# Kernel optimization log

Measured on AMD Instinct MI355X. Metric: run time of the kernel, lower is better.

Reference implementation:

```python
import jax, jax.numpy as jnp
import numpy as np

H = 24; W = 24; N = H * W            # board tokens
R = 4; BINS = (2 * R + 1) ** 2 + 1    # 82 rel-pos bins (far bin = 81)
G = 2                                  # num_global_tokens
T = N + 1 + G                          # cls + globals + board tokens = 579
D = 256; NH = 8; HD = D // NH
DEPTH = 6; MLP = int(D * 2.0)
B = 16; CIN = 10


def _ln(x, g, b):
    m = jnp.mean(x, axis=-1, keepdims=True)
    v = jnp.mean(jnp.square(x - m), axis=-1, keepdims=True)
    return (x - m) * jax.lax.rsqrt(v + 1e-5) * g + b


def _head(x, g, b, w1, b1, w2, b2):
    h = _ln(x, g, b)
    h = jax.nn.gelu(h @ w1 + b1, approximate=False)
    return h @ w2 + b2


def _forward(obs, input_w, input_b, cls_token, global_tokens, row_embed, col_embed,
             ln1_g, ln1_b, qkv_w, qkv_b, proj_w, proj_b, rel_bias,
             ln2_g, ln2_b, fc1_w, fc1_b, fc2_w, fc2_b,
             norm_g, norm_b,
             pol_ln_g, pol_ln_b, pol_w1, pol_b1, pol_w2, pol_b2,
             val_ln_g, val_ln_b, val_w1, val_b1, val_w2, val_b2,
             rel_idx):
    Bsz = obs.shape[0]
    # _tokens_from_obs: (B, C, H, W) -> (B, N, C); channel order is already [revealed, counts]
    tokens = obs.reshape(Bsz, CIN, N).transpose(0, 2, 1)
    x = tokens @ input_w + input_b                                    # (B, N, D)
    pos = (row_embed[:, None, :] + col_embed[None, :, :]).reshape(N, D)
    x = x + pos
    x = jnp.concatenate([jnp.broadcast_to(cls_token, (Bsz, 1, D)),
                         jnp.broadcast_to(global_tokens, (Bsz, G, D)),
                         x], axis=1)                                   # (B, T, D)
    scale = 1.0 / jnp.sqrt(jnp.float32(HD))

    def block(x, p):
        l1g, l1b, qw, qb, pw, pb, rb, l2g, l2b, f1w, f1b, f2w, f2b = p
        h = _ln(x, l1g, l1b)
        qkv = (h @ qw + qb).reshape(Bsz, T, 3, NH, HD)
        q, k, v = qkv[:, :, 0], qkv[:, :, 1], qkv[:, :, 2]             # (B, T, NH, HD)
        bias = rb[:, rel_idx]                                          # (NH, T, T) gathered bias
        scores = jnp.einsum('bqhd,bkhd->bhqk', q, k) * scale + bias[None]
        probs = jax.nn.softmax(scores, axis=-1)
        o = jnp.einsum('bhqk,bkhd->bqhd', probs, v).reshape(Bsz, T, D)
        x = x + o @ pw + pb
        h2 = _ln(x, l2g, l2b)
        x = x + jax.nn.gelu(h2 @ f1w + f1b, approximate=False) @ f2w + f2b
        return x, None

    params = (ln1_g, ln1_b, qkv_w, qkv_b, proj_w, proj_b, rel_bias,
              ln2_g, ln2_b, fc1_w, fc1_b, fc2_w, fc2_b)
    x, _ = jax.lax.scan(block, x, params)
    x = _ln(x, norm_g, norm_b)
    cls_tok = x[:, 0]
    token_states = x[:, 1:N + 1]   # faithful to source slice (includes the global tokens)
    logits = _head(token_states, pol_ln_g, pol_ln_b, pol_w1, pol_b1, pol_w2, pol_b2)[..., 0]  # (B, N)
    value = _head(cls_tok, val_ln_g, val_ln_b, val_w1, val_b1, val_w2, val_b2)                 # (B, 1)
    return jnp.concatenate([logits, value], axis=1)  # (B, N+1)


def setup_inputs() -> dict:
    keys = iter(jax.random.split(jax.random.key(0), 40))
    def p(shape, s=0.02):
        return jax.random.normal(next(keys), shape, jnp.float32) * s
    # _build_rel_pos_index, embedded into full (T, T) buffer with far_bin elsewhere
    coords = np.stack(np.meshgrid(np.arange(H), np.arange(W), indexing='ij'), -1).reshape(-1, 2)
    rel = coords[:, None, :] - coords[None, :, :]
    far = (np.abs(rel) > R).any(-1)
    rel = np.clip(rel, -R, R) + R
    idx = rel[..., 0] * (2 * R + 1) + rel[..., 1]
    idx = np.where(far, BINS - 1, idx)
    full = np.full((T, T), BINS - 1, np.int32)
    full[1:N + 1, 1:N + 1] = idx
    return {
        'obs': jax.random.normal(next(keys), (B, CIN, H, W), jnp.float32),
        'input_w': p((CIN, D)), 'input_b': jnp.zeros((D,)),
        'cls_token': jnp.zeros((1, 1, D)),
        'global_tokens': jnp.zeros((1, G, D)),
        'row_embed': p((H, D)), 'col_embed': p((W, D)),
        'ln1_g': jnp.ones((DEPTH, D)), 'ln1_b': jnp.zeros((DEPTH, D)),
        'qkv_w': p((DEPTH, D, 3 * D)), 'qkv_b': jnp.zeros((DEPTH, 3 * D)),
        'proj_w': p((DEPTH, D, D)), 'proj_b': jnp.zeros((DEPTH, D)),
        'rel_bias': p((DEPTH, NH, BINS)),
        'ln2_g': jnp.ones((DEPTH, D)), 'ln2_b': jnp.zeros((DEPTH, D)),
        'fc1_w': p((DEPTH, D, MLP)), 'fc1_b': jnp.zeros((DEPTH, MLP)),
        'fc2_w': p((DEPTH, MLP, D)), 'fc2_b': jnp.zeros((DEPTH, D)),
        'norm_g': jnp.ones((D,)), 'norm_b': jnp.zeros((D,)),
        'pol_ln_g': jnp.ones((D,)), 'pol_ln_b': jnp.zeros((D,)),
        'pol_w1': p((D, D)), 'pol_b1': jnp.zeros((D,)),
        'pol_w2': p((D, 1)), 'pol_b2': jnp.zeros((1,)),
        'val_ln_g': jnp.ones((D,)), 'val_ln_b': jnp.zeros((D,)),
        'val_w1': p((D, D)), 'val_b1': jnp.zeros((D,)),
        'val_w2': p((D, 1)), 'val_b2': jnp.zeros((1,)),
        'rel_idx': jnp.asarray(full),
    }


def reference(obs, input_w, input_b, cls_token, global_tokens, row_embed, col_embed,
              ln1_g, ln1_b, qkv_w, qkv_b, proj_w, proj_b, rel_bias,
              ln2_g, ln2_b, fc1_w, fc1_b, fc2_w, fc2_b,
              norm_g, norm_b,
              pol_ln_g, pol_ln_b, pol_w1, pol_b1, pol_w2, pol_b2,
              val_ln_g, val_ln_b, val_w1, val_b1, val_w2, val_b2,
              rel_idx):
    return _forward(obs, input_w, input_b, cls_token, global_tokens, row_embed, col_embed,
                    ln1_g, ln1_b, qkv_w, qkv_b, proj_w, proj_b, rel_bias,
                    ln2_g, ln2_b, fc1_w, fc1_b, fc2_w, fc2_b,
                    norm_g, norm_b,
                    pol_ln_g, pol_ln_b, pol_w1, pol_b1, pol_w2, pol_b2,
                    val_ln_g, val_ln_b, val_w1, val_b1, val_w2, val_b2,
                    rel_idx)
```

## Files before the change

kernel.cpp:

```cpp
#include <hip/hip_runtime.h>
#include <math.h>

constexpr int Hc = 24, Wc = 24, Nc = 576, BINSc = 82, Gc = 2;
constexpr int Tc = Nc + 1 + Gc;
constexpr int Dc = 256, NHc = 8, HDc = 32, DEPTHc = 6, MLPc = 512;
constexpr int Bc = 16, CINc = 10;
constexpr int BT = Bc * Tc;
constexpr float SCALE = 0.17677669529663687f;

typedef _Float16 f16;
typedef _Float16 f16x8 __attribute__((ext_vector_type(8)));
typedef _Float16 f16x16 __attribute__((ext_vector_type(16)));
typedef float f32x4 __attribute__((ext_vector_type(4)));

constexpr size_t QK_ST   = (size_t)BT * 256;
constexpr int    VT_PAD  = 640;
constexpr size_t VT_ST   = (size_t)Bc * NHc * 32 * VT_PAD;
constexpr size_t OFF_KH  = 2 * QK_ST;
constexpr size_t OFF_VTH = 4 * QK_ST;
constexpr size_t OFF_BIAS = 4 * QK_ST + 2 * VT_ST;
constexpr int    BPAD    = 580;
constexpr size_t R_F16   = OFF_BIAS + (size_t)NHc * Tc * BPAD;
constexpr size_t R_FLOATS = 8707904;

__device__ __forceinline__ int xcd_swz(int d, int nwg) {
    const int q = nwg >> 3, r = nwg & 7;
    const int x = d & 7, s = d >> 3;
    return x * q + (x < r ? x : r) + s;
}

__device__ __forceinline__ float gelu_f(float x) {
    return 0.5f * x * (1.0f + erff(x * 0.70710678118654752f));
}

__device__ __forceinline__ float block_sum256(float v, float* s4) {
    #pragma unroll
    for (int off = 32; off > 0; off >>= 1) v += __shfl_down(v, off, 64);
    __syncthreads();
    if ((threadIdx.x & 63) == 0) s4[threadIdx.x >> 6] = v;
    __syncthreads();
    return s4[0] + s4[1] + s4[2] + s4[3];
}

__global__ __launch_bounds__(256) void embed_kernel(
        const float* __restrict__ obs, const float* __restrict__ iw,
        const float* __restrict__ ib, const float* __restrict__ cls,
        const float* __restrict__ glob, const float* __restrict__ rowe,
        const float* __restrict__ cole, float* __restrict__ x) {
    int t = blockIdx.x, b = blockIdx.y, d = threadIdx.x;
    float v;
    if (t == 0) {
        v = cls[d];
    } else if (t <= Gc) {
        v = glob[(t - 1) * Dc + d];
    } else {
        int n = t - 1 - Gc;
        float acc = ib[d];
        #pragma unroll
        for (int c = 0; c < CINc; ++c)
            acc = fmaf(obs[(b * CINc + c) * Nc + n], iw[c * Dc + d], acc);
        v = acc + rowe[(n / Wc) * Dc + d] + cole[(n % Wc) * Dc + d];
    }
    x[((size_t)b * Tc + t) * Dc + d] = v;
}

__global__ __launch_bounds__(256) void lnstats_kernel(
        const float* __restrict__ x, float2* __restrict__ st, int nrows) {
    const int w = threadIdx.x >> 6, l = threadIdx.x & 63;
    const int row = blockIdx.x * 4 + w;
    if (row >= nrows) return;
    const float4 v = *reinterpret_cast<const float4*>(x + (size_t)row * Dc + l * 4);
    float s = v.x + v.y + v.z + v.w;
    #pragma unroll
    for (int mk = 1; mk < 64; mk <<= 1) s += __shfl_xor(s, mk, 64);
    const float m = s * (1.0f / 256.0f);
    float vs = (v.x - m) * (v.x - m) + (v.y - m) * (v.y - m) +
               (v.z - m) * (v.z - m) + (v.w - m) * (v.w - m);
    #pragma unroll
    for (int mk = 1; mk < 64; mk <<= 1) vs += __shfl_xor(vs, mk, 64);
    if (l == 0)
        st[row] = make_float2(m, rsqrtf(vs * (1.0f / 256.0f) + 1e-5f));
}

__global__ __launch_bounds__(256) void ln4_kernel(
        const float* __restrict__ x, const float* __restrict__ g,
        const float* __restrict__ b, float* __restrict__ out, int nrows) {
    const int w = threadIdx.x >> 6, l = threadIdx.x & 63;
    const int row = blockIdx.x * 4 + w;
    if (row >= nrows) return;
    const float4 v = *reinterpret_cast<const float4*>(x + (size_t)row * Dc + l * 4);
    float s = v.x + v.y + v.z + v.w;
    #pragma unroll
    for (int mk = 1; mk < 64; mk <<= 1) s += __shfl_xor(s, mk, 64);
    const float m = s * (1.0f / 256.0f);
    const float4 d = make_float4(v.x - m, v.y - m, v.z - m, v.w - m);
    float vs = d.x * d.x + d.y * d.y + d.z * d.z + d.w * d.w;
    #pragma unroll
    for (int mk = 1; mk < 64; mk <<= 1) vs += __shfl_xor(vs, mk, 64);
    const float rs = rsqrtf(vs * (1.0f / 256.0f) + 1e-5f);
    const float4 gg = *reinterpret_cast<const float4*>(g + l * 4);
    const float4 bb = *reinterpret_cast<const float4*>(b + l * 4);
    *reinterpret_cast<float4*>(out + (size_t)row * Dc + l * 4) =
        make_float4(d.x * rs * gg.x + bb.x, d.y * rs * gg.y + bb.y,
                    d.z * rs * gg.z + bb.z, d.w * rs * gg.w + bb.w);
}

__global__ __launch_bounds__(256) void lnsel4_kernel(
        const float* __restrict__ xn, const float* __restrict__ g,
        const float* __restrict__ b, float* __restrict__ out) {
    const int w = threadIdx.x >> 6, l = threadIdx.x & 63;
    const int rr = blockIdx.x * 4 + w;
    const int bb = rr / Nc, n = rr % Nc;
    const float* xr = xn + ((size_t)bb * Tc + 1 + n) * Dc;
    const float4 v = *reinterpret_cast<const float4*>(xr + l * 4);
    float s = v.x + v.y + v.z + v.w;
    #pragma unroll
    for (int mk = 1; mk < 64; mk <<= 1) s += __shfl_xor(s, mk, 64);
    const float m = s * (1.0f / 256.0f);
    const float4 d = make_float4(v.x - m, v.y - m, v.z - m, v.w - m);
    float vs = d.x * d.x + d.y * d.y + d.z * d.z + d.w * d.w;
    #pragma unroll
    for (int mk = 1; mk < 64; mk <<= 1) vs += __shfl_xor(vs, mk, 64);
    const float rs = rsqrtf(vs * (1.0f / 256.0f) + 1e-5f);
    const float4 gg = *reinterpret_cast<const float4*>(g + l * 4);
    const float4 bb4 = *reinterpret_cast<const float4*>(b + l * 4);
    *reinterpret_cast<float4*>(out + ((size_t)bb * Nc + n) * Dc + l * 4) =
        make_float4(d.x * rs * gg.x + bb4.x, d.y * rs * gg.y + bb4.y,
                    d.z * rs * gg.z + bb4.z, d.w * rs * gg.w + bb4.w);
}

__global__ __launch_bounds__(256) void split_w_kernel(
        const float* __restrict__ qkv_w, const float* __restrict__ proj_w,
        const float* __restrict__ fc1_w, const float* __restrict__ fc2_w,
        const float* __restrict__ pol_w1, f16* __restrict__ out) {
    int r = blockIdx.x * 256 + threadIdx.x;
    float v; f16* dst; int NK;
    if (r < 1179648) {
        int layer = r / 196608, e = r % 196608;
        int n = e >> 8, k = e & 255;
        v = qkv_w[(size_t)layer * 196608 + k * 768 + n];
        dst = out + (size_t)layer * 393216 + n * 256 + k; NK = 196608;
    } else if (r < 1572864) {
        int rr = r - 1179648; int layer = rr / 65536, e = rr % 65536;
        int n = e >> 8, k = e & 255;
        v = proj_w[(size_t)layer * 65536 + k * 256 + n];
        dst = out + 2359296 + (size_t)layer * 131072 + n * 256 + k; NK = 65536;
    } else if (r < 2359296) {
        int rr = r - 1572864; int layer = rr / 131072, e = rr % 131072;
        int n = e >> 8, k = e & 255;
        v = fc1_w[(size_t)layer * 131072 + k * 512 + n];
        dst = out + 3145728 + (size_t)layer * 262144 + n * 256 + k; NK = 131072;
    } else if (r < 3145728) {
        int rr = r - 2359296; int layer = rr / 131072, e = rr % 131072;
        int n = e >> 9, k = e & 511;
        v = fc2_w[(size_t)layer * 131072 + k * 256 + n];
        dst = out + 4718592 + (size_t)layer * 262144 + n * 512 + k; NK = 131072;
    } else if (r < 3211264) {
        int rr = r - 3145728; int n = rr >> 8, k = rr & 255;
        v = pol_w1[k * 256 + n];
        dst = out + 6291456 + n * 256 + k; NK = 65536;
    } else return;
    f16 h = (f16)v;
    dst[0] = h;
    dst[NK] = (f16)(v - (float)h);
}

__global__ __launch_bounds__(256) void biasgen_kernel(
        const float* __restrict__ relb, const int* __restrict__ relidx,
        f16* __restrict__ bias) {
    const int q = blockIdx.x, h = blockIdx.y;
    const size_t rowo = ((size_t)h * Tc + q) * BPAD;
    const int* ridx = relidx + q * Tc;
    const float* rb = relb + h * BINSc;
    for (int kp = threadIdx.x; kp * 2 + 1 < Tc; kp += 256) {
        f16 b0 = (f16)rb[ridx[kp * 2]];
        f16 b1 = (f16)rb[ridx[kp * 2 + 1]];
        unsigned pk = (unsigned)__builtin_bit_cast(unsigned short, b0) |
                      ((unsigned)__builtin_bit_cast(unsigned short, b1) << 16);
        *reinterpret_cast<unsigned*>(&bias[rowo + kp * 2]) = pk;
    }
    if (threadIdx.x == 0)
        bias[rowo + Tc - 1] = (f16)rb[ridx[Tc - 1]];
}

__device__ __forceinline__ int swz(int r, int g) {
    return r * 40 + ((g ^ ((r >> 3) & 3)) << 3);
}
template <int ACT, bool RES, bool LNA>
__global__ __launch_bounds__(256) void mgemm_kernel(
        const float* __restrict__ A, const f16* __restrict__ WT,
        const float* __restrict__ bias, const float* __restrict__ res,
        float* __restrict__ C, int M, int N, int K, int nbx,
        const float2* __restrict__ lnst, const float* __restrict__ lng,
        const float* __restrict__ lnb) {
    constexpr int BM = 128, BN = 64, BK = 32;
    __shared__ f16 Ah[BM * 40], Al[BM * 40];
    __shared__ f16 Bh[BN * 40], Bl[BN * 40];
    const int tid = threadIdx.x;
    const int v = xcd_swz(blockIdx.x, gridDim.x);
    const int m0 = (v / nbx) * BM, n0 = (v % nbx) * BN;
    const int w = tid >> 6, l = tid & 63;
    const int wm = (w >> 1) * 64, wn = (w & 1) * 32;
    const int lg = l >> 4, lr = l & 15;
    f32x4 acc[4][2] = {};
    const int sa_row = tid >> 1, sa_kc = (tid & 1) * 16;
    const int sb_part = tid >> 7;
    const int sb_n = (tid & 127) >> 1, sb_kc = (tid & 1) * 16;

    int gr = m0 + sa_row; if (gr >= M) gr = M - 1;
    float mu = 0.f, rsd = 1.f;
    if constexpr (LNA) { float2 s2 = lnst[gr]; mu = s2.x; rsd = s2.y; }

    for (int k0 = 0; k0 < K; k0 += BK) {
        {
            const float4* src = reinterpret_cast<const float4*>(
                A + (size_t)gr * K + k0 + sa_kc);
            f16x8 hv0, hv1, lv0, lv1;
            #pragma unroll
            for (int c = 0; c < 4; ++c) {
                float4 v4 = src[c];
                if constexpr (LNA) {
                    const float4 g4 = *reinterpret_cast<const float4*>(
                        lng + k0 + sa_kc + c * 4);
                    const float4 b4 = *reinterpret_cast<const float4*>(
                        lnb + k0 + sa_kc + c * 4);
                    v4.x = (v4.x - mu) * rsd * g4.x + b4.x;
                    v4.y = (v4.y - mu) * rsd * g4.y + b4.y;
                    v4.z = (v4.z - mu) * rsd * g4.z + b4.z;
                    v4.w = (v4.w - mu) * rsd * g4.w + b4.w;
                }
                f16 h0 = (f16)v4.x, h1 = (f16)v4.y, h2 = (f16)v4.z, h3 = (f16)v4.w;
                f16 l0 = (f16)(v4.x - (float)h0), l1 = (f16)(v4.y - (float)h1);
                f16 l2 = (f16)(v4.z - (float)h2), l3 = (f16)(v4.w - (float)h3);
                if (c < 2) {
                    hv0[c * 4 + 0] = h0; hv0[c * 4 + 1] = h1;
                    hv0[c * 4 + 2] = h2; hv0[c * 4 + 3] = h3;
                    lv0[c * 4 + 0] = l0; lv0[c * 4 + 1] = l1;
                    lv0[c * 4 + 2] = l2; lv0[c * 4 + 3] = l3;
                } else {
                    hv1[(c - 2) * 4 + 0] = h0; hv1[(c - 2) * 4 + 1] = h1;
                    hv1[(c - 2) * 4 + 2] = h2; hv1[(c - 2) * 4 + 3] = h3;
                    lv1[(c - 2) * 4 + 0] = l0; lv1[(c - 2) * 4 + 1] = l1;
                    lv1[(c - 2) * 4 + 2] = l2; lv1[(c - 2) * 4 + 3] = l3;
                }
            }
            const int g0 = sa_kc >> 3;
            *reinterpret_cast<f16x8*>(&Ah[swz(sa_row, g0)])     = hv0;
            *reinterpret_cast<f16x8*>(&Ah[swz(sa_row, g0 + 1)]) = hv1;
            *reinterpret_cast<f16x8*>(&Al[swz(sa_row, g0)])     = lv0;
            *reinterpret_cast<f16x8*>(&Al[swz(sa_row, g0 + 1)]) = lv1;
        }
        {
            const f16x8* src = reinterpret_cast<const f16x8*>(
                WT + (size_t)sb_part * N * K + (size_t)(n0 + sb_n) * K + k0 + sb_kc);
            f16* dbase = sb_part ? Bl : Bh;
            const int g0 = sb_kc >> 3;
            *reinterpret_cast<f16x8*>(&dbase[swz(sb_n, g0)])     = src[0];
            *reinterpret_cast<f16x8*>(&dbase[swz(sb_n, g0 + 1)]) = src[1];
        }
        __syncthreads();
        f16x8 afh[4], afl[4], bfh[2], bfl[2];
        #pragma unroll
        for (int mi = 0; mi < 4; ++mi) {
            int row = wm + mi * 16 + lr;
            afh[mi] = *reinterpret_cast<const f16x8*>(&Ah[swz(row, lg)]);
            afl[mi] = *reinterpret_cast<const f16x8*>(&Al[swz(row, lg)]);
        }
        #pragma unroll
        for (int ni = 0; ni < 2; ++ni) {
            int col = wn + ni * 16 + lr;
            bfh[ni] = *reinterpret_cast<const f16x8*>(&Bh[swz(col, lg)]);
            bfl[ni] = *reinterpret_cast<const f16x8*>(&Bl[swz(col, lg)]);
        }
        #pragma unroll
        for (int mi = 0; mi < 4; ++mi)
            #pragma unroll
            for (int ni = 0; ni < 2; ++ni) {
                acc[mi][ni] = __builtin_amdgcn_mfma_f32_16x16x32_f16(
                    afh[mi], bfh[ni], acc[mi][ni], 0, 0, 0);
                acc[mi][ni] = __builtin_amdgcn_mfma_f32_16x16x32_f16(
                    afh[mi], bfl[ni], acc[mi][ni], 0, 0, 0);
                acc[mi][ni] = __builtin_amdgcn_mfma_f32_16x16x32_f16(
                    afl[mi], bfh[ni], acc[mi][ni], 0, 0, 0);
            }
        __syncthreads();
    }
    float bv[2];
    #pragma unroll
    for (int ni = 0; ni < 2; ++ni) bv[ni] = bias[n0 + wn + ni * 16 + lr];
    #pragma unroll
    for (int mi = 0; mi < 4; ++mi) {
        #pragma unroll
        for (int r = 0; r < 4; ++r) {
            int grow = m0 + wm + mi * 16 + lg * 4 + r;
            if (grow >= M) continue;
            if constexpr (ACT == 2) {
                f16* base = (f16*)C;
                const int bb = grow / Tc;
                const int tt = grow - bb * Tc;
                #pragma unroll
                for (int ni = 0; ni < 2; ++ni) {
                    const int gcol = n0 + wn + ni * 16 + lr;
                    float vv = acc[mi][ni][r] + bv[ni];
                    if (gcol < 256) {
                        vv *= SCALE;
                        f16 hh = (f16)vv;
                        base[(size_t)grow * 256 + gcol] = hh;
                        base[QK_ST + (size_t)grow * 256 + gcol] = (f16)(vv - (float)hh);
                    } else if (gcol < 512) {
                        f16 hh = (f16)vv;
                        base[OFF_KH + (size_t)grow * 256 + (gcol - 256)] = hh;
                        base[OFF_KH + QK_ST + (size_t)grow * 256 + (gcol - 256)] =
                            (f16)(vv - (float)hh);
                    } else {
                        const int e = gcol - 512;
                        const int hh_ = e >> 5, dd = e & 31;
                        const size_t o =
                            ((size_t)((bb * NHc + hh_) * 32 + dd)) * VT_PAD + tt;
                        f16 hh = (f16)vv;
                        base[OFF_VTH + o] = hh;
                        base[OFF_VTH + VT_ST + o] = (f16)(vv - (float)hh);
                    }
                }
            } else {
                #pragma unroll
                for (int ni = 0; ni < 2; ++ni) {
                    int gcol = n0 + wn + ni * 16 + lr;
                    float vv = acc[mi][ni][r] + bv[ni];
                    if (ACT == 1) vv = gelu_f(vv);
                    if (RES) vv += res[(size_t)grow * N + gcol];
                    C[(size_t)grow * N + gcol] = vv;
                }
            }
        }
    }
}

__global__ __launch_bounds__(256, 4) void mattn2_kernel(
        const f16* __restrict__ qsp, float* __restrict__ o) {
    __shared__ __align__(16) f16 Kh_s[64][40], Kl_s[64][40];
    __shared__ __align__(16) f16 VTh_s[32][72], VTl_s[32][72];
    __shared__ __align__(16) f16 Ph_s[4][16][72], Pl_s[4][16][72];
    const f16* __restrict__ Kh_g  = qsp + OFF_KH;
    const f16* __restrict__ VTh_g = qsp + OFF_VTH;
    const f16* __restrict__ bias_g = qsp + OFF_BIAS;

    const int tid = threadIdx.x;
    const int v = xcd_swz(blockIdx.x, 1280);
    const int h = v / 160;
    const int rem = v - h * 160;
    const int b = rem / 10, qt = rem - b * 10;
    const int q0 = qt * 64;
    const int w = tid >> 6, l = tid & 63;
    const int lr = l & 15, lg = l >> 4;

    int qrow = q0 + w * 16 + lr; if (qrow >= Tc) qrow = Tc - 1;
    const f16* qp = qsp + ((size_t)(b * Tc + qrow)) * 256 + h * 32 + lg * 8;
    const f16x8 Qh = *reinterpret_cast<const f16x8*>(qp);
    const f16x8 Ql = *reinterpret_cast<const f16x8*>(qp + QK_ST);
    const int myq = q0 + w * 16 + lg * 4;

    int boff[4];
    #pragma unroll
    for (int r = 0; r < 4; ++r) {
        int qq = myq + r; if (qq >= Tc) qq = Tc - 1;
        boff[r] = (h * Tc + qq) * BPAD;
    }

    const int skrow = tid >> 2, skc = (tid & 3) * 8;
    const int svd = tid >> 3, svc = (tid & 7) * 8;
    const f16* vrow = VTh_g + ((size_t)((b * NHc + h) * 32 + svd)) * VT_PAD;

    struct KV { f16x8 kh, kl, vh, vl; };
    auto load_kv = [&](int k0) {
        KV r;
        int gk = k0 + skrow; if (gk >= Tc) gk = Tc - 1;
        const f16* kp = Kh_g + ((size_t)(b * Tc + gk)) * 256 + h * 32 + skc;
        r.kh = *reinterpret_cast<const f16x8*>(kp);
        r.kl = *reinterpret_cast<const f16x8*>(kp + QK_ST);
        const f16* vp = vrow + k0 + svc;
        r.vh = *reinterpret_cast<const f16x8*>(vp);
        r.vl = *reinterpret_cast<const f16x8*>(vp + VT_ST);
        return r;
    };
    auto load_bias = [&](int k0) {
        f16x16 bv;
        #pragma unroll
        for (int r = 0; r < 4; ++r)
            #pragma unroll
            for (int j = 0; j < 4; ++j) {
                int kk = k0 + j * 16 + lr; if (kk >= Tc) kk = Tc - 1;
                bv[r * 4 + j] = bias_g[boff[r] + kk];
            }
        return bv;
    };

    KV pA = load_kv(0);
    KV pB = load_kv(64);
    f16x16 bias_c = load_bias(0), bias_n;

    f16x8 kOnes;
    #pragma unroll
    for (int e = 0; e < 8; ++e) kOnes[e] = (f16)1.0f;

    float m_run[4];
    f32x4 Oacc[2] = {};
    f32x4 Oext = {};
    #pragma unroll
    for (int r = 0; r < 4; ++r) m_run[r] = -1e30f;

    for (int t = 0; t < 10; ++t) {
        const int k0 = t * 64;
        __syncthreads();
        *reinterpret_cast<f16x8*>(&Kh_s[skrow][skc]) = pA.kh;
        *reinterpret_cast<f16x8*>(&Kl_s[skrow][skc]) = pA.kl;
        *reinterpret_cast<f16x8*>(&VTh_s[svd][svc]) = pA.vh;
        *reinterpret_cast<f16x8*>(&VTl_s[svd][svc]) = pA.vl;
        pA = pB;
        if (t + 2 < 10) pB = load_kv(k0 + 128);
        __syncthreads();
        if (t + 1 < 10) bias_n = load_bias(k0 + 64);
        f32x4 sc[4];
        #pragma unroll
        for (int j = 0; j < 4; ++j) {
            const f16x8 kh = *reinterpret_cast<const f16x8*>(&Kh_s[j * 16 + lr][lg * 8]);
            const f16x8 kl = *reinterpret_cast<const f16x8*>(&Kl_s[j * 16 + lr][lg * 8]);
            f32x4 s = {(float)bias_c[j], (float)bias_c[4 + j],
                       (float)bias_c[8 + j], (float)bias_c[12 + j]};
            s = __builtin_amdgcn_mfma_f32_16x16x32_f16(Qh, kh, s, 0, 0, 0);
            s = __builtin_amdgcn_mfma_f32_16x16x32_f16(Qh, kl, s, 0, 0, 0);
            s = __builtin_amdgcn_mfma_f32_16x16x32_f16(Ql, kh, s, 0, 0, 0);
            sc[j] = s;
        }
        #pragma unroll
        for (int j = 0; j < 4; ++j) {
            const int kk = k0 + j * 16 + lr;
            if (kk >= Tc) { sc[j][0] = sc[j][1] = sc[j][2] = sc[j][3] = -1e30f; }
        }
        #pragma unroll
        for (int r = 0; r < 4; ++r) {
            float tm = fmaxf(fmaxf(sc[0][r], sc[1][r]), fmaxf(sc[2][r], sc[3][r]));
            #pragma unroll
            for (int mk = 1; mk < 16; mk <<= 1) tm = fmaxf(tm, __shfl_xor(tm, mk, 64));
            const float mn = fmaxf(m_run[r], tm);
            const float resc = __expf(m_run[r] - mn);
            m_run[r] = mn;
            Oacc[0][r] *= resc; Oacc[1][r] *= resc; Oext[r] *= resc;
            const int prow = lg * 4 + r;
            #pragma unroll
            for (int j = 0; j < 4; ++j) {
                const float p = __expf(sc[j][r] - mn);
                const f16 ph = (f16)p;
                Ph_s[w][prow][j * 16 + lr] = ph;
                Pl_s[w][prow][j * 16 + lr] = (f16)(p - (float)ph);
            }
        }
        #pragma unroll
        for (int kc = 0; kc < 2; ++kc) {
            const f16x8 Pa = *reinterpret_cast<const f16x8*>(&Ph_s[w][lr][kc * 32 + lg * 8]);
            const f16x8 Pb = *reinterpret_cast<const f16x8*>(&Pl_s[w][lr][kc * 32 + lg * 8]);
            #pragma unroll
            for (int dt = 0; dt < 2; ++dt) {
                const f16x8 vh = *reinterpret_cast<const f16x8*>(&VTh_s[dt * 16 + lr][kc * 32 + lg * 8]);
                const f16x8 vl = *reinterpret_cast<const f16x8*>(&VTl_s[dt * 16 + lr][kc * 32 + lg * 8]);
                Oacc[dt] = __builtin_amdgcn_mfma_f32_16x16x32_f16(Pa, vh, Oacc[dt], 0, 0, 0);
                Oacc[dt] = __builtin_amdgcn_mfma_f32_16x16x32_f16(Pa, vl, Oacc[dt], 0, 0, 0);
                Oacc[dt] = __builtin_amdgcn_mfma_f32_16x16x32_f16(Pb, vh, Oacc[dt], 0, 0, 0);
            }
            Oext = __builtin_amdgcn_mfma_f32_16x16x32_f16(Pa, kOnes, Oext, 0, 0, 0);
            Oext = __builtin_amdgcn_mfma_f32_16x16x32_f16(Pb, kOnes, Oext, 0, 0, 0);
        }
        if (t + 1 < 10) bias_c = bias_n;
    }
    #pragma unroll
    for (int r = 0; r < 4; ++r) {
        const int qq = myq + r;
        if (qq < Tc) {
            const float inv = 1.0f / Oext[r];
            float* op = o + ((size_t)b * Tc + qq) * Dc + h * HDc;
            op[lr]      = Oacc[0][r] * inv;
            op[16 + lr] = Oacc[1][r] * inv;
        }
    }
}

__global__ __launch_bounds__(256) void logits_kernel(
        const float* __restrict__ ph, const float* __restrict__ w2,
        const float* __restrict__ b2, float* __restrict__ out) {
    __shared__ float s4[4];
    size_t r = blockIdx.x;
    int bb = (int)(r / Nc), n = (int)(r % Nc);
    float v = ph[r * Dc + threadIdx.x] * w2[threadIdx.x];
    float s = block_sum256(v, s4);
    if (threadIdx.x == 0) out[bb * (Nc + 1) + n] = s + b2[0];
}

__global__ __launch_bounds__(256) void value_kernel(
        const float* __restrict__ xn, const float* __restrict__ g,
        const float* __restrict__ b, const float* __restrict__ w1,
        const float* __restrict__ b1, const float* __restrict__ w2,
        const float* __restrict__ b2, float* __restrict__ out) {
    __shared__ float s4[4];
    __shared__ float ts[Dc];
    const int bb = blockIdx.x, tid = threadIdx.x;
    float v = xn[(size_t)bb * Tc * Dc + tid];
    float m = block_sum256(v, s4) * (1.0f / 256.0f);
    float d = v - m;
    float var = block_sum256(d * d, s4) * (1.0f / 256.0f);
    ts[tid] = d * rsqrtf(var + 1e-5f) * g[tid] + b[tid];
    __syncthreads();
    float acc = b1[tid];
    #pragma unroll 8
    for (int i = 0; i < Dc; ++i) acc = fmaf(ts[i], w1[i * Dc + tid], acc);
    float hv = gelu_f(acc) * w2[tid];
    float s = block_sum256(hv, s4);
    if (tid == 0) out[bb * (Nc + 1) + Nc] = s + b2[0];
}

extern "C" void kernel_launch(void* const* d_in, const int* in_sizes, int n_in,
                              void* d_out, int out_size, void* d_ws, size_t ws_size,
                              hipStream_t stream) {
    const float* obs      = (const float*)d_in[0];
    const float* input_w  = (const float*)d_in[1];
    const float* input_b  = (const float*)d_in[2];
    const float* cls_tok  = (const float*)d_in[3];
    const float* glob_tok = (const float*)d_in[4];
    const float* row_emb  = (const float*)d_in[5];
    const float* col_emb  = (const float*)d_in[6];
    const float* ln1_g    = (const float*)d_in[7];
    const float* ln1_b    = (const float*)d_in[8];
    const float* qkv_w    = (const float*)d_in[9];
    const float* qkv_b    = (const float*)d_in[10];
    const float* proj_w   = (const float*)d_in[11];
    const float* proj_b   = (const float*)d_in[12];
    const float* rel_bias = (const float*)d_in[13];
    const float* ln2_g    = (const float*)d_in[14];
    const float* ln2_b    = (const float*)d_in[15];
    const float* fc1_w    = (const float*)d_in[16];
    const float* fc1_b    = (const float*)d_in[17];
    const float* fc2_w    = (const float*)d_in[18];
    const float* fc2_b    = (const float*)d_in[19];
    const float* norm_g   = (const float*)d_in[20];
    const float* norm_b   = (const float*)d_in[21];
    const float* pol_ln_g = (const float*)d_in[22];
    const float* pol_ln_b = (const float*)d_in[23];
    const float* pol_w1   = (const float*)d_in[24];
    const float* pol_b1   = (const float*)d_in[25];
    const float* pol_w2   = (const float*)d_in[26];
    const float* pol_b2   = (const float*)d_in[27];
    const float* val_ln_g = (const float*)d_in[28];
    const float* val_ln_b = (const float*)d_in[29];
    const float* val_w1   = (const float*)d_in[30];
    const float* val_b1   = (const float*)d_in[31];
    const float* val_w2   = (const float*)d_in[32];
    const float* val_b2   = (const float*)d_in[33];
    const int*   rel_idx  = (const int*)d_in[34];
    float* out = (float*)d_out;

    float* ws = (float*)d_ws;
    const size_t SZ_XD = (size_t)BT * Dc;
    float* X  = ws;
    float* Hb = ws + SZ_XD;
    float* R  = ws + 2 * SZ_XD;
    f16* qsp = (f16*)R;
    f16* bias_g = qsp + OFF_BIAS;
    float* MLPH = R;
    float* PT = R;
    float* PH = R + (size_t)Bc * Nc * Dc;
    f16* wsplit = (f16*)(R + R_FLOATS);
    float2* lnst = (float2*)(wsplit + 6422528);

    auto qkvT = [&](int l) { return wsplit + (size_t)l * 393216; };
    auto projT = [&](int l) { return wsplit + 2359296 + (size_t)l * 131072; };
    auto fc1T = [&](int l) { return wsplit + 3145728 + (size_t)l * 262144; };
    auto fc2T = [&](int l) { return wsplit + 4718592 + (size_t)l * 262144; };
    f16* polT = wsplit + 6291456;

    split_w_kernel<<<12544, 256, 0, stream>>>(
        qkv_w, proj_w, fc1_w, fc2_w, pol_w1, wsplit);

    embed_kernel<<<dim3(Tc, Bc), 256, 0, stream>>>(
        obs, input_w, input_b, cls_tok, glob_tok, row_emb, col_emb, X);

    for (int l = 0; l < DEPTHc; ++l) {
        lnstats_kernel<<<(BT + 3) / 4, 256, 0, stream>>>(X, lnst, BT);
        mgemm_kernel<2, false, true><<<876, 256, 0, stream>>>(
            X, qkvT(l), qkv_b + l * 3 * Dc, nullptr, (float*)qsp, BT, 3 * Dc, Dc, 12,
            lnst, ln1_g + l * Dc, ln1_b + l * Dc);
        biasgen_kernel<<<dim3(Tc, NHc), 256, 0, stream>>>(
            rel_bias + l * NHc * BINSc, rel_idx, bias_g);
        mattn2_kernel<<<1280, 256, 0, stream>>>(qsp, Hb);
        mgemm_kernel<0, true, false><<<292, 256, 0, stream>>>(
            Hb, projT(l), proj_b + l * Dc, X, X, BT, Dc, Dc, 4,
            nullptr, nullptr, nullptr);
        lnstats_kernel<<<(BT + 3) / 4, 256, 0, stream>>>(X, lnst, BT);
        mgemm_kernel<1, false, true><<<584, 256, 0, stream>>>(
            X, fc1T(l), fc1_b + l * MLPc, nullptr, MLPH, BT, MLPc, Dc, 8,
            lnst, ln2_g + l * Dc, ln2_b + l * Dc);
        mgemm_kernel<0, true, false><<<292, 256, 0, stream>>>(
            MLPH, fc2T(l), fc2_b + l * Dc, X, X, BT, Dc, MLPc, 4,
            nullptr, nullptr, nullptr);
    }

    ln4_kernel<<<(BT + 3) / 4, 256, 0, stream>>>(X, norm_g, norm_b, Hb, BT);
    lnsel4_kernel<<<Bc * Nc / 4, 256, 0, stream>>>(Hb, pol_ln_g, pol_ln_b, PT);
    mgemm_kernel<1, false, false><<<288, 256, 0, stream>>>(
        PT, polT, pol_b1, nullptr, PH, Bc * Nc, Dc, Dc, 4,
        nullptr, nullptr, nullptr);
    logits_kernel<<<Bc * Nc, 256, 0, stream>>>(PH, pol_w2, pol_b2, out);
    value_kernel<<<Bc, 256, 0, stream>>>(
        Hb, val_ln_g, val_ln_b, val_w1, val_b1, val_w2, val_b2, out);
}
```

Measured before the change: 1.300 ms.

## Pre-split GEMM A operands into fp16 hi/lo in producers instead of per-tile

LayerNorm, attention output and fc1 GELU output now write fp16 hi/lo split pairs directly, so downstream GEMMs load ready-made f16 tiles instead of reading fp32 and splitting (and normalizing) inside every column-block tile. This removes redundant per-N-tile conversion work and halves nothing in bytes but avoids repeated LN math across 12/8 column blocks. The final norm and the policy/value head LNs are fused into single kernels, and workspace layout is reshuffled. It adds an extra full-size write pass for LN outputs in exchange for cheaper GEMM A-loads.

New measurement: 1.195 ms. 8.1% less time.

```diff
diff --git a/kernel.cpp b/kernel.cpp
--- a/kernel.cpp
+++ b/kernel.cpp
@@ -9,6 +9,7 @@
 constexpr float SCALE = 0.17677669529663687f;
 
 typedef _Float16 f16;
+typedef _Float16 f16x4 __attribute__((ext_vector_type(4)));
 typedef _Float16 f16x8 __attribute__((ext_vector_type(8)));
 typedef _Float16 f16x16 __attribute__((ext_vector_type(16)));
 typedef float f32x4 __attribute__((ext_vector_type(4)));
@@ -64,30 +65,11 @@
     x[((size_t)b * Tc + t) * Dc + d] = v;
 }
 
-__global__ __launch_bounds__(256) void lnstats_kernel(
-        const float* __restrict__ x, float2* __restrict__ st, int nrows) {
+__global__ __launch_bounds__(256) void splitA_ln_kernel(
+        const float* __restrict__ x, const float* __restrict__ g,
+        const float* __restrict__ b, f16* __restrict__ outp) {
     const int w = threadIdx.x >> 6, l = threadIdx.x & 63;
     const int row = blockIdx.x * 4 + w;
-    if (row >= nrows) return;
-    const float4 v = *reinterpret_cast<const float4*>(x + (size_t)row * Dc + l * 4);
-    float s = v.x + v.y + v.z + v.w;
-    #pragma unroll
-    for (int mk = 1; mk < 64; mk <<= 1) s += __shfl_xor(s, mk, 64);
-    const float m = s * (1.0f / 256.0f);
-    float vs = (v.x - m) * (v.x - m) + (v.y - m) * (v.y - m) +
-               (v.z - m) * (v.z - m) + (v.w - m) * (v.w - m);
-    #pragma unroll
-    for (int mk = 1; mk < 64; mk <<= 1) vs += __shfl_xor(vs, mk, 64);
-    if (l == 0)
-        st[row] = make_float2(m, rsqrtf(vs * (1.0f / 256.0f) + 1e-5f));
-}
-
-__global__ __launch_bounds__(256) void ln4_kernel(
-        const float* __restrict__ x, const float* __restrict__ g,
-        const float* __restrict__ b, float* __restrict__ out, int nrows) {
-    const int w = threadIdx.x >> 6, l = threadIdx.x & 63;
-    const int row = blockIdx.x * 4 + w;
-    if (row >= nrows) return;
     const float4 v = *reinterpret_cast<const float4*>(x + (size_t)row * Dc + l * 4);
     float s = v.x + v.y + v.z + v.w;
     #pragma unroll
@@ -100,33 +82,52 @@
     const float rs = rsqrtf(vs * (1.0f / 256.0f) + 1e-5f);
     const float4 gg = *reinterpret_cast<const float4*>(g + l * 4);
     const float4 bb = *reinterpret_cast<const float4*>(b + l * 4);
-    *reinterpret_cast<float4*>(out + (size_t)row * Dc + l * 4) =
-        make_float4(d.x * rs * gg.x + bb.x, d.y * rs * gg.y + bb.y,
-                    d.z * rs * gg.z + bb.z, d.w * rs * gg.w + bb.w);
-}
-
-__global__ __launch_bounds__(256) void lnsel4_kernel(
-        const float* __restrict__ xn, const float* __restrict__ g,
-        const float* __restrict__ b, float* __restrict__ out) {
+    const float y0 = d.x * rs * gg.x + bb.x, y1 = d.y * rs * gg.y + bb.y;
+    const float y2 = d.z * rs * gg.z + bb.z, y3 = d.w * rs * gg.w + bb.w;
+    const f16 h0 = (f16)y0, h1 = (f16)y1, h2 = (f16)y2, h3 = (f16)y3;
+    f16x4 hv = {h0, h1, h2, h3};
+    f16x4 lv = {(f16)(y0 - (float)h0), (f16)(y1 - (float)h1),
+                (f16)(y2 - (float)h2), (f16)(y3 - (float)h3)};
+    *reinterpret_cast<f16x4*>(outp + (size_t)row * Dc + l * 4) = hv;
+    *reinterpret_cast<f16x4*>(outp + QK_ST + (size_t)row * Dc + l * 4) = lv;
+}
+
+__global__ __launch_bounds__(256) void lnself_kernel(
+        const float* __restrict__ X, const float* __restrict__ ng,
+        const float* __restrict__ nb, const float* __restrict__ pg,
+        const float* __restrict__ pb, float* __restrict__ out) {
     const int w = threadIdx.x >> 6, l = threadIdx.x & 63;
     const int rr = blockIdx.x * 4 + w;
     const int bb = rr / Nc, n = rr % Nc;
-    const float* xr = xn + ((size_t)bb * Tc + 1 + n) * Dc;
+    const float* xr = X + ((size_t)bb * Tc + 1 + n) * Dc;
     const float4 v = *reinterpret_cast<const float4*>(xr + l * 4);
     float s = v.x + v.y + v.z + v.w;
     #pragma unroll
     for (int mk = 1; mk < 64; mk <<= 1) s += __shfl_xor(s, mk, 64);
     const float m = s * (1.0f / 256.0f);
-    const float4 d = make_float4(v.x - m, v.y - m, v.z - m, v.w - m);
+    float4 d = make_float4(v.x - m, v.y - m, v.z - m, v.w - m);
     float vs = d.x * d.x + d.y * d.y + d.z * d.z + d.w * d.w;
     #pragma unroll
     for (int mk = 1; mk < 64; mk <<= 1) vs += __shfl_xor(vs, mk, 64);
     const float rs = rsqrtf(vs * (1.0f / 256.0f) + 1e-5f);
-    const float4 gg = *reinterpret_cast<const float4*>(g + l * 4);
-    const float4 bb4 = *reinterpret_cast<const float4*>(b + l * 4);
+    const float4 gg = *reinterpret_cast<const float4*>(ng + l * 4);
+    const float4 bb4 = *reinterpret_cast<const float4*>(nb + l * 4);
+    float4 y = make_float4(d.x * rs * gg.x + bb4.x, d.y * rs * gg.y + bb4.y,
+                           d.z * rs * gg.z + bb4.z, d.w * rs * gg.w + bb4.w);
+    float s2 = y.x + y.y + y.z + y.w;
+    #pragma unroll
+    for (int mk = 1; mk < 64; mk <<= 1) s2 += __shfl_xor(s2, mk, 64);
+    const float m2 = s2 * (1.0f / 256.0f);
+    float4 d2 = make_float4(y.x - m2, y.y - m2, y.z - m2, y.w - m2);
+    float vs2 = d2.x * d2.x + d2.y * d2.y + d2.z * d2.z + d2.w * d2.w;
+    #pragma unroll
+    for (int mk = 1; mk < 64; mk <<= 1) vs2 += __shfl_xor(vs2, mk, 64);
+    const float rs2 = rsqrtf(vs2 * (1.0f / 256.0f) + 1e-5f);
+    const float4 pg4 = *reinterpret_cast<const float4*>(pg + l * 4);
+    const float4 pb4 = *reinterpret_cast<const float4*>(pb + l * 4);
     *reinterpret_cast<float4*>(out + ((size_t)bb * Nc + n) * Dc + l * 4) =
-        make_float4(d.x * rs * gg.x + bb4.x, d.y * rs * gg.y + bb4.y,
-                    d.z * rs * gg.z + bb4.z, d.w * rs * gg.w + bb4.w);
+        make_float4(d2.x * rs2 * pg4.x + pb4.x, d2.y * rs2 * pg4.y + pb4.y,
+                    d2.z * rs2 * pg4.z + pb4.z, d2.w * rs2 * pg4.w + pb4.w);
 }
 
 __global__ __launch_bounds__(256) void split_w_kernel(
@@ -186,13 +187,11 @@
 __device__ __forceinline__ int swz(int r, int g) {
     return r * 40 + ((g ^ ((r >> 3) & 3)) << 3);
 }
-template <int ACT, bool RES, bool LNA>
+template <int ACT, bool RES, bool PSA>
 __global__ __launch_bounds__(256) void mgemm_kernel(
-        const float* __restrict__ A, const f16* __restrict__ WT,
+        const void* __restrict__ Ap, const f16* __restrict__ WT,
         const float* __restrict__ bias, const float* __restrict__ res,
-        float* __restrict__ C, int M, int N, int K, int nbx,
-        const float2* __restrict__ lnst, const float* __restrict__ lng,
-        const float* __restrict__ lnb) {
+        void* __restrict__ Cp, int M, int N, int K, int nbx, size_t osplit) {
     constexpr int BM = 128, BN = 64, BK = 32;
     __shared__ f16 Ah[BM * 40], Al[BM * 40];
     __shared__ f16 Bh[BN * 40], Bl[BN * 40];
@@ -208,27 +207,28 @@
     const int sb_n = (tid & 127) >> 1, sb_kc = (tid & 1) * 16;
 
     int gr = m0 + sa_row; if (gr >= M) gr = M - 1;
-    float mu = 0.f, rsd = 1.f;
-    if constexpr (LNA) { float2 s2 = lnst[gr]; mu = s2.x; rsd = s2.y; }
 
     for (int k0 = 0; k0 < K; k0 += BK) {
-        {
+        const int g0 = sa_kc >> 3;
+        if constexpr (PSA) {
+            const f16* Ah_g = (const f16*)Ap;
+            const f16* src = Ah_g + (size_t)gr * K + k0 + sa_kc;
+            *reinterpret_cast<f16x8*>(&Ah[swz(sa_row, g0)]) =
+                *reinterpret_cast<const f16x8*>(src);
+            *reinterpret_cast<f16x8*>(&Ah[swz(sa_row, g0 + 1)]) =
+                *reinterpret_cast<const f16x8*>(src + 8);
+            const f16* srcl = src + (size_t)M * K;
+            *reinterpret_cast<f16x8*>(&Al[swz(sa_row, g0)]) =
+                *reinterpret_cast<const f16x8*>(srcl);
+            *reinterpret_cast<f16x8*>(&Al[swz(sa_row, g0 + 1)]) =
+                *reinterpret_cast<const f16x8*>(srcl + 8);
+        } else {
             const float4* src = reinterpret_cast<const float4*>(
-                A + (size_t)gr * K + k0 + sa_kc);
+                (const float*)Ap + (size_t)gr * K + k0 + sa_kc);
             f16x8 hv0, hv1, lv0, lv1;
             #pragma unroll
             for (int c = 0; c < 4; ++c) {
                 float4 v4 = src[c];
-                if constexpr (LNA) {
-                    const float4 g4 = *reinterpret_cast<const float4*>(
-                        lng + k0 + sa_kc + c * 4);
-                    const float4 b4 = *reinterpret_cast<const float4*>(
-                        lnb + k0 + sa_kc + c * 4);
-                    v4.x = (v4.x - mu) * rsd * g4.x + b4.x;
-                    v4.y = (v4.y - mu) * rsd * g4.y + b4.y;
-                    v4.z = (v4.z - mu) * rsd * g4.z + b4.z;
-                    v4.w = (v4.w - mu) * rsd * g4.w + b4.w;
-                }
                 f16 h0 = (f16)v4.x, h1 = (f16)v4.y, h2 = (f16)v4.z, h3 = (f16)v4.w;
                 f16 l0 = (f16)(v4.x - (float)h0), l1 = (f16)(v4.y - (float)h1);
                 f16 l2 = (f16)(v4.z - (float)h2), l3 = (f16)(v4.w - (float)h3);
@@ -244,7 +244,6 @@
                     lv1[(c - 2) * 4 + 2] = l2; lv1[(c - 2) * 4 + 3] = l3;
                 }
             }
-            const int g0 = sa_kc >> 3;
             *reinterpret_cast<f16x8*>(&Ah[swz(sa_row, g0)])     = hv0;
             *reinterpret_cast<f16x8*>(&Ah[swz(sa_row, g0 + 1)]) = hv1;
             *reinterpret_cast<f16x8*>(&Al[swz(sa_row, g0)])     = lv0;
@@ -254,9 +253,9 @@
             const f16x8* src = reinterpret_cast<const f16x8*>(
                 WT + (size_t)sb_part * N * K + (size_t)(n0 + sb_n) * K + k0 + sb_kc);
             f16* dbase = sb_part ? Bl : Bh;
-            const int g0 = sb_kc >> 3;
-            *reinterpret_cast<f16x8*>(&dbase[swz(sb_n, g0)])     = src[0];
-            *reinterpret_cast<f16x8*>(&dbase[swz(sb_n, g0 + 1)]) = src[1];
+            const int gb = sb_kc >> 3;
+            *reinterpret_cast<f16x8*>(&dbase[swz(sb_n, gb)])     = src[0];
+            *reinterpret_cast<f16x8*>(&dbase[swz(sb_n, gb + 1)]) = src[1];
         }
         __syncthreads();
         f16x8 afh[4], afl[4], bfh[2], bfl[2];
@@ -295,7 +294,7 @@
             int grow = m0 + wm + mi * 16 + lg * 4 + r;
             if (grow >= M) continue;
             if constexpr (ACT == 2) {
-                f16* base = (f16*)C;
+                f16* base = (f16*)Cp;
                 const int bb = grow / Tc;
                 const int tt = grow - bb * Tc;
                 #pragma unroll
@@ -322,7 +321,18 @@
                         base[OFF_VTH + VT_ST + o] = (f16)(vv - (float)hh);
                     }
                 }
+            } else if constexpr (ACT == 3) {
+                f16* base = (f16*)Cp;
+                #pragma unroll
+                for (int ni = 0; ni < 2; ++ni) {
+                    const int gcol = n0 + wn + ni * 16 + lr;
+                    float vv = gelu_f(acc[mi][ni][r] + bv[ni]);
+                    f16 hh = (f16)vv;
+                    base[(size_t)grow * N + gcol] = hh;
+                    base[osplit + (size_t)grow * N + gcol] = (f16)(vv - (float)hh);
+                }
             } else {
+                float* C = (float*)Cp;
                 #pragma unroll
                 for (int ni = 0; ni < 2; ++ni) {
                     int gcol = n0 + wn + ni * 16 + lr;
@@ -337,7 +347,7 @@
 }
 
 __global__ __launch_bounds__(256, 4) void mattn2_kernel(
-        const f16* __restrict__ qsp, float* __restrict__ o) {
+        const f16* __restrict__ qsp, f16* __restrict__ ao) {
     __shared__ __align__(16) f16 Kh_s[64][40], Kl_s[64][40];
     __shared__ __align__(16) f16 VTh_s[32][72], VTl_s[32][72];
     __shared__ __align__(16) f16 Ph_s[4][16][72], Pl_s[4][16][72];
@@ -477,9 +487,14 @@
         const int qq = myq + r;
         if (qq < Tc) {
             const float inv = 1.0f / Oext[r];
-            float* op = o + ((size_t)b * Tc + qq) * Dc + h * HDc;
-            op[lr]      = Oacc[0][r] * inv;
-            op[16 + lr] = Oacc[1][r] * inv;
+            const float v0 = Oacc[0][r] * inv, v1 = Oacc[1][r] * inv;
+            const f16 h0 = (f16)v0, h1 = (f16)v1;
+            f16* op = ao + ((size_t)b * Tc + qq) * 256 + h * HDc;
+            op[lr] = h0;
+            op[16 + lr] = h1;
+            f16* ol = op + QK_ST;
+            ol[lr] = (f16)(v0 - (float)h0);
+            ol[16 + lr] = (f16)(v1 - (float)h1);
         }
     }
 }
@@ -496,18 +511,23 @@
 }
 
 __global__ __launch_bounds__(256) void value_kernel(
-        const float* __restrict__ xn, const float* __restrict__ g,
+        const float* __restrict__ X, const float* __restrict__ ng,
+        const float* __restrict__ nb, const float* __restrict__ g,
         const float* __restrict__ b, const float* __restrict__ w1,
         const float* __restrict__ b1, const float* __restrict__ w2,
         const float* __restrict__ b2, float* __restrict__ out) {
     __shared__ float s4[4];
     __shared__ float ts[Dc];
     const int bb = blockIdx.x, tid = threadIdx.x;
-    float v = xn[(size_t)bb * Tc * Dc + tid];
+    float v = X[(size_t)bb * Tc * Dc + tid];
     float m = block_sum256(v, s4) * (1.0f / 256.0f);
     float d = v - m;
     float var = block_sum256(d * d, s4) * (1.0f / 256.0f);
-    ts[tid] = d * rsqrtf(var + 1e-5f) * g[tid] + b[tid];
+    float y = d * rsqrtf(var + 1e-5f) * ng[tid] + nb[tid];
+    float m2 = block_sum256(y, s4) * (1.0f / 256.0f);
+    float d2 = y - m2;
+    float var2 = block_sum256(d2 * d2, s4) * (1.0f / 256.0f);
+    ts[tid] = d2 * rsqrtf(var2 + 1e-5f) * g[tid] + b[tid];
     __syncthreads();
     float acc = b1[tid];
     #pragma unroll 8
@@ -560,15 +580,14 @@
     float* ws = (float*)d_ws;
     const size_t SZ_XD = (size_t)BT * Dc;
     float* X  = ws;
-    float* Hb = ws + SZ_XD;
-    float* R  = ws + 2 * SZ_XD;
+    float* R  = ws + SZ_XD;
     f16* qsp = (f16*)R;
     f16* bias_g = qsp + OFF_BIAS;
-    float* MLPH = R;
+    f16* Mh = qsp;
+    f16* Aq = (f16*)(R + R_FLOATS);
+    f16* wsplit = (f16*)(R + R_FLOATS + SZ_XD);
     float* PT = R;
-    float* PH = R + (size_t)Bc * Nc * Dc;
-    f16* wsplit = (f16*)(R + R_FLOATS);
-    float2* lnst = (float2*)(wsplit + 6422528);
+    float* PH = (float*)wsplit;
 
     auto qkvT = [&](int l) { return wsplit + (size_t)l * 393216; };
     auto projT = [&](int l) { return wsplit + 2359296 + (size_t)l * 131072; };
@@ -583,31 +602,29 @@
         obs, input_w, input_b, cls_tok, glob_tok, row_emb, col_emb, X);
 
     for (int l = 0; l < DEPTHc; ++l) {
-        lnstats_kernel<<<(BT + 3) / 4, 256, 0, stream>>>(X, lnst, BT);
+        splitA_ln_kernel<<<BT / 4, 256, 0, stream>>>(
+            X, ln1_g + l * Dc, ln1_b + l * Dc, Aq);
         mgemm_kernel<2, false, true><<<876, 256, 0, stream>>>(
-            X, qkvT(l), qkv_b + l * 3 * Dc, nullptr, (float*)qsp, BT, 3 * Dc, Dc, 12,
-            lnst, ln1_g + l * Dc, ln1_b + l * Dc);
+            Aq, qkvT(l), qkv_b + l * 3 * Dc, nullptr, qsp, BT, 3 * Dc, Dc, 12, 0);
         biasgen_kernel<<<dim3(Tc, NHc), 256, 0, stream>>>(
             rel_bias + l * NHc * BINSc, rel_idx, bias_g);
-        mattn2_kernel<<<1280, 256, 0, stream>>>(qsp, Hb);
-        mgemm_kernel<0, true, false><<<292, 256, 0, stream>>>(
-            Hb, projT(l), proj_b + l * Dc, X, X, BT, Dc, Dc, 4,
-            nullptr, nullptr, nullptr);
-        lnstats_kernel<<<(BT + 3) / 4, 256, 0, stream>>>(X, lnst, BT);
-        mgemm_kernel<1, false, true><<<584, 256, 0, stream>>>(
-            X, fc1T(l), fc1_b + l * MLPc, nullptr, MLPH, BT, MLPc, Dc, 8,
-            lnst, ln2_g + l * Dc, ln2_b + l * Dc);
-        mgemm_kernel<0, true, false><<<292, 256, 0, stream>>>(
-            MLPH, fc2T(l), fc2_b + l * Dc, X, X, BT, Dc, MLPc, 4,
-            nullptr, nullptr, nullptr);
-    }
-
-    ln4_kernel<<<(BT + 3) / 4, 256, 0, stream>>>(X, norm_g, norm_b, Hb, BT);
-    lnsel4_kernel<<<Bc * Nc / 4, 256, 0, stream>>>(Hb, pol_ln_g, pol_ln_b, PT);
+        mattn2_kernel<<<1280, 256, 0, stream>>>(qsp, Aq);
+        mgemm_kernel<0, true, true><<<292, 256, 0, stream>>>(
+            Aq, projT(l), proj_b + l * Dc, X, X, BT, Dc, Dc, 4, 0);
+        splitA_ln_kernel<<<BT / 4, 256, 0, stream>>>(
+            X, ln2_g + l * Dc, ln2_b + l * Dc, Aq);
+        mgemm_kernel<3, false, true><<<584, 256, 0, stream>>>(
+            Aq, fc1T(l), fc1_b + l * MLPc, nullptr, Mh, BT, MLPc, Dc, 8,
+            (size_t)BT * MLPc);
+        mgemm_kernel<0, true, true><<<292, 256, 0, stream>>>(
+            Mh, fc2T(l), fc2_b + l * Dc, X, X, BT, Dc, MLPc, 4, 0);
+    }
+
+    lnself_kernel<<<Bc * Nc / 4, 256, 0, stream>>>(
+        X, norm_g, norm_b, pol_ln_g, pol_ln_b, PT);
     mgemm_kernel<1, false, false><<<288, 256, 0, stream>>>(
-        PT, polT, pol_b1, nullptr, PH, Bc * Nc, Dc, Dc, 4,
-        nullptr, nullptr, nullptr);
+        PT, polT, pol_b1, nullptr, PH, Bc * Nc, Dc, Dc, 4, 0);
     logits_kernel<<<Bc * Nc, 256, 0, stream>>>(PH, pol_w2, pol_b2, out);
     value_kernel<<<Bc, 256, 0, stream>>>(
-        Hb, val_ln_g, val_ln_b, val_w1, val_b1, val_w2, val_b2, out);
-}
+        X, norm_g, norm_b, val_ln_g, val_ln_b, val_w1, val_b1, val_w2, val_b2, out);
+}
```
